# Optimization experiments

Hardware: AMD Instinct MI355X
Metric: run time of the kernel (lower is better)

The kernel has to match this reference:

```python
import jax, jax.numpy as jnp
import numpy as np

NUM_NODES = 50000
NUM_RELATIONS = 16
NUM_EDGES = 800000
HIDDEN = 64
NUM_CLASSES = 16


def setup_inputs() -> dict:
    key = jax.random.key(0)
    ks = jax.random.split(key, 8)
    edge_index = jax.random.randint(ks[0], (2, NUM_EDGES), 0, NUM_NODES, dtype=jnp.int32)
    edge_type = jax.random.randint(ks[1], (NUM_EDGES,), 0, NUM_RELATIONS, dtype=jnp.int32)
    node_emb = jax.random.normal(ks[2], (NUM_NODES, HIDDEN), dtype=jnp.float32) * 0.1
    W1 = jax.random.normal(ks[3], (NUM_RELATIONS, HIDDEN, HIDDEN), dtype=jnp.float32) * 0.1
    root1 = jax.random.normal(ks[4], (HIDDEN, HIDDEN), dtype=jnp.float32) * 0.1
    b1 = jnp.zeros((HIDDEN,), dtype=jnp.float32)
    W2 = jax.random.normal(ks[5], (NUM_RELATIONS, HIDDEN, NUM_CLASSES), dtype=jnp.float32) * 0.1
    root2 = jax.random.normal(ks[6], (HIDDEN, NUM_CLASSES), dtype=jnp.float32) * 0.1
    b2 = jnp.zeros((NUM_CLASSES,), dtype=jnp.float32)
    return {"edge_index": edge_index, "edge_type": edge_type, "node_emb": node_emb,
            "W1": W1, "root1": root1, "b1": b1, "W2": W2, "root2": root2, "b2": b2}


def rgcn_conv(x, src, dst, edge_type, W, root, bias, num_nodes):
    # PyG RGCNConv (aggr='mean', root_weight=True, bias=True, num_bases=None):
    # per relation r: transform all nodes, gather at src, scatter-MEAN at dst
    # (mean over edges of that relation per target node); sum over relations;
    # then add root transform and bias.
    out_dim = W.shape[-1]

    def body(acc, rw):
        W_r, r = rw
        h = x @ W_r                                   # [N, out]
        mask = (edge_type == r).astype(x.dtype)       # [E]
        msg = h[src] * mask[:, None]                  # [E, out]
        summed = jax.ops.segment_sum(msg, dst, num_segments=num_nodes)  # [N, out]
        cnt = jax.ops.segment_sum(mask, dst, num_segments=num_nodes)    # [N]
        mean = jnp.where(cnt[:, None] > 0, summed / jnp.maximum(cnt, 1.0)[:, None], 0.0)
        return acc + mean, None

    acc0 = jnp.zeros((num_nodes, out_dim), dtype=x.dtype)
    agg, _ = jax.lax.scan(body, acc0, (W, jnp.arange(W.shape[0])))
    return agg + x @ root + bias


def reference(edge_index, edge_type, node_emb, W1, root1, b1, W2, root2, b2):
    src, dst = edge_index[0], edge_index[1]
    n = node_emb.shape[0]
    x = rgcn_conv(node_emb, src, dst, edge_type, W1, root1, b1, n)
    x = jax.nn.relu(x)  # dropout p=0.0 -> identity
    x = rgcn_conv(x, src, dst, edge_type, W2, root2, b2, n)
    return x
```

## Files before the change

kernel.cpp:

```cpp
#include <hip/hip_runtime.h>
#include <hip/hip_bf16.h>

#define N_NODES 50000
#define NREL 16
#define HID 64
#define NCLS 16
#define NBKT (N_NODES * NREL)
#define SB 2048
#define NSB ((NBKT + SB - 1) / SB)
#define TILE 32
#define NTB ((N_NODES + TILE - 1) / TILE)
#define PGRID 256
#define XCHUNKS (N_NODES * HID / 8)
#define W1N (17 * HID * HID)
#define W2N (17 * NCLS * HID)

typedef __attribute__((ext_vector_type(8))) short bf16x8;
typedef __attribute__((ext_vector_type(4))) float f32x4;
typedef __attribute__((ext_vector_type(2))) int i32x2;

static __device__ __forceinline__ unsigned short f2bf(float f) {
    __hip_bfloat16 h = __float2bfloat16(f);
    return *reinterpret_cast<unsigned short*>(&h);
}
static __device__ __forceinline__ float bf2f(unsigned short u) {
    __hip_bfloat16 h;
    *reinterpret_cast<unsigned short*>(&h) = u;
    return __bfloat162float(h);
}

#define MFMA16(A, B, C) __builtin_amdgcn_mfma_f32_16x16x32_bf16((A), (B), (C), 0, 0, 0)

#define LD128A(D, P) \
    asm volatile("global_load_dwordx4 %0, %1, off" : "=v"(D) : "v"((const void*)(P)) : "memory")
#define LD64A(D, P) \
    asm volatile("global_load_dwordx2 %0, %1, off" : "=v"(D) : "v"((const void*)(P)) : "memory")
#define VWAIT0()                                           \
    do {                                                   \
        asm volatile("s_waitcnt vmcnt(0)" ::: "memory");   \
        __builtin_amdgcn_sched_barrier(0);                 \
    } while (0)


__global__ __launch_bounds__(256) void pre_k(const int* __restrict__ dstp,
                                             const int* __restrict__ et,
                                             int* __restrict__ bcnt, int E,
                                             const float* __restrict__ x,
                                             const float* __restrict__ W1,
                                             const float* __restrict__ root1,
                                             const float* __restrict__ W2,
                                             const float* __restrict__ root2,
                                             ushort* __restrict__ xb,
                                             ushort* __restrict__ WbT1,
                                             ushort* __restrict__ WbT2) {
    int eb = (E + 255) >> 8;
    if ((int)blockIdx.x < eb) {
        int i = blockIdx.x * 256 + threadIdx.x;
        if (i < E) atomicAdd(&bcnt[dstp[i] * NREL + et[i]], 1);
        return;
    }
    int i = (blockIdx.x - eb) * 256 + threadIdx.x;
    if (i < XCHUNKS) {
        float4 f0 = *(const float4*)(x + (size_t)i * 8);
        float4 f1 = *(const float4*)(x + (size_t)i * 8 + 4);
        bf16x8 o;
        o[0] = (short)f2bf(f0.x); o[1] = (short)f2bf(f0.y);
        o[2] = (short)f2bf(f0.z); o[3] = (short)f2bf(f0.w);
        o[4] = (short)f2bf(f1.x); o[5] = (short)f2bf(f1.y);
        o[6] = (short)f2bf(f1.z); o[7] = (short)f2bf(f1.w);
        *(bf16x8*)(xb + (size_t)i * 8) = o;
    } else {
        int j = i - XCHUNKS;
        if (j < W1N) {
            int t = j >> 12, rem = j & 4095, n = rem >> 6, k = rem & 63;
            float v = (t < 16) ? W1[(size_t)t * HID * HID + k * HID + n]
                               : root1[k * HID + n];
            WbT1[j] = f2bf(v);
        } else {
            int m = j - W1N;
            if (m < W2N) {
                int t = m >> 10, rem = m & 1023, n = rem >> 6, k = rem & 63;
                float v = (t < 16) ? W2[(size_t)t * HID * NCLS + k * NCLS + n]
                                   : root2[k * NCLS + n];
                WbT2[m] = f2bf(v);
            }
        }
    }
}

__global__ __launch_bounds__(256) void scan1_k(const int* __restrict__ bcnt,
                                               int* __restrict__ bsum) {
    int b = blockIdx.x, t = threadIdx.x;
    int base = b * SB + t * 8;
    int s = 0;
#pragma unroll
    for (int j = 0; j < 8; ++j)
        if (base + j < NBKT) s += bcnt[base + j];
#pragma unroll
    for (int off = 1; off < 64; off <<= 1) s += __shfl_xor(s, off, 64);
    __shared__ int ws[4];
    if ((t & 63) == 0) ws[t >> 6] = s;
    __syncthreads();
    if (t == 0) bsum[b] = ws[0] + ws[1] + ws[2] + ws[3];
}

__global__ __launch_bounds__(256) void scan23_k(int* __restrict__ bcnt,
                                                const int* __restrict__ bsum,
                                                int* __restrict__ cursor, int E) {
    int b = blockIdx.x, t = threadIdx.x;
    int ps = 0;
    for (int j = t; j < b; j += 256) ps += bsum[j];
#pragma unroll
    for (int off = 1; off < 64; off <<= 1) ps += __shfl_xor(ps, off, 64);
    __shared__ int wps[4];
    __shared__ int prefix;
    if ((t & 63) == 0) wps[t >> 6] = ps;
    __syncthreads();
    if (t == 0) prefix = wps[0] + wps[1] + wps[2] + wps[3];

    int base = b * SB + t * 8;
    int a[8];
    int s = 0;
#pragma unroll
    for (int j = 0; j < 8; ++j) {
        a[j] = (base + j < NBKT) ? bcnt[base + j] : 0;
        s += a[j];
    }
    __shared__ int ts[256];
    ts[t] = s;
    __syncthreads();
    int acc = s;
    for (int off = 1; off < 256; off <<= 1) {
        int u = (t >= off) ? ts[t - off] : 0;
        __syncthreads();
        acc += u;
        ts[t] = acc;
        __syncthreads();
    }
    int run = prefix + (acc - s);
#pragma unroll
    for (int j = 0; j < 8; ++j) {
        if (base + j < NBKT) {
            bcnt[base + j] = run;
            cursor[base + j] = run;
        }
        run += a[j];
    }
    if (b == 0 && t == 0) bcnt[NBKT] = E;
}

__global__ __launch_bounds__(256) void scat_k(const int* __restrict__ srcp,
                                              const int* __restrict__ dstp,
                                              const int* __restrict__ et,
                                              const int* __restrict__ rstart,
                                              int* __restrict__ cursor,
                                              int2* __restrict__ sedge, int E) {
    int i = blockIdx.x * 256 + threadIdx.x;
    if (i < E) {
        int r = et[i];
        int b = dstp[i] * NREL + r;
        int p = atomicAdd(&cursor[b], 1);
        float inv = 1.0f / (float)(rstart[b + 1] - rstart[b]);
        sedge[p] = make_int2(srcp[i] | (r << 16), __float_as_int(inv));
    }
}


#define RSTART_LOAD(T, LO, HI)                                                \
    do {                                                                      \
        int node_ = (T) * TILE + g;                                           \
        LO = 0; HI = 0;                                                       \
        if (node_ < N_NODES) {                                                \
            int b0_ = node_ * NREL + h * 8;                                   \
            LO = rstart[b0_];                                                 \
            HI = rstart[b0_ + 8];                                             \
        }                                                                     \
    } while (0)

#define DESC_ISSUE(LO, HI)                                                    \
    do {                                                                      \
        int dg_ = (HI) - (LO);                                                \
        int bs_ = dg_ > 0 ? (LO) : 0;                                         \
        int lt_ = dg_ > 0 ? (HI)-1 : 0;                                       \
        _Pragma("unroll") for (int j_ = 0; j_ < 16; ++j_) {                   \
            int ix_ = bs_ + j_;                                               \
            if (ix_ > lt_) ix_ = lt_;                                         \
            LD64A(d[j_], sedge + ix_);                                        \
        }                                                                     \
    } while (0)

#define FEAT_ISSUE()                                                          \
    do {                                                                      \
        _Pragma("unroll") for (int j_ = 0; j_ < 16; ++j_)                     \
            LD128A(v[j_], xcol + (size_t)(d[j_].x & 0xFFFF) * HID);           \
    } while (0)

#define GFLUSHX(ABP)                                                          \
    {                                                                         \
        bf16x8 o_;                                                            \
        o_[0] = (short)f2bf(acc_[0]); o_[1] = (short)f2bf(acc_[1]);           \
        o_[2] = (short)f2bf(acc_[2]); o_[3] = (short)f2bf(acc_[3]);           \
        o_[4] = (short)f2bf(acc_[4]); o_[5] = (short)f2bf(acc_[5]);           \
        o_[6] = (short)f2bf(acc_[6]); o_[7] = (short)f2bf(acc_[7]);           \
        *(bf16x8*)((ABP) + ((curRel_ * (TILE * 128) + rowoff) ^ swg)) = o_;   \
        acc_[0] = 0.f; acc_[1] = 0.f; acc_[2] = 0.f; acc_[3] = 0.f;           \
        acc_[4] = 0.f; acc_[5] = 0.f; acc_[6] = 0.f; acc_[7] = 0.f;           \
    }

#define CONSUME(ABP, LO, HI)                                                  \
    do {                                                                      \
        char* abp_ = (char*)(ABP);                                            \
        int deg_ = (HI) - (LO);                                               \
        const bf16x8 zz_ = {0, 0, 0, 0, 0, 0, 0, 0};                          \
        _Pragma("unroll") for (int r_ = 0; r_ < 8; ++r_)                      \
            *(bf16x8*)(abp_ + (((h * 8 + r_) * (TILE * 128) + rowoff) ^ swg)) = zz_; \
        float acc_[8] = {0.f, 0.f, 0.f, 0.f, 0.f, 0.f, 0.f, 0.f};             \
        int curRel_ = h * 8;                                                  \
        _Pragma("unroll") for (int j_ = 0; j_ < 16; ++j_) {                   \
            if (j_ < deg_) {                                                  \
                int rr_ = (d[j_].x >> 16) & 15;                               \
                if (rr_ != curRel_) { GFLUSHX(abp_); curRel_ = rr_; }         \
                float iv_ = __int_as_float(d[j_].y);                          \
                _Pragma("unroll") for (int q_ = 0; q_ < 8; ++q_)              \
                    acc_[q_] = fmaf(iv_, bf2f((unsigned short)v[j_][q_]), acc_[q_]); \
            }                                                                 \
        }                                                                     \
        for (int e_ = (LO) + 16; e_ < (HI); ++e_) {            \
            int2 m_ = sedge[e_];                                              \
            int rr_ = (m_.x >> 16) & 15;                                      \
            if (rr_ != curRel_) { GFLUSHX(abp_); curRel_ = rr_; }             \
            float iv_ = __int_as_float(m_.y);                                 \
            bf16x8 vv_ = *(const bf16x8*)(xcol + (size_t)(m_.x & 0xFFFF) * HID); \
            _Pragma("unroll") for (int q_ = 0; q_ < 8; ++q_)                  \
                acc_[q_] = fmaf(iv_, bf2f((unsigned short)vv_[q_]), acc_[q_]); \
        }                                                                     \
        if (deg_ > 0) GFLUSHX(abp_);                                          \
    } while (0)

__global__ __launch_bounds__(512, 2) void fuse1_k(const ushort* __restrict__ xb,
                                                  const int2* __restrict__ sedge,
                                                  const int* __restrict__ rstart,
                                                  const ushort* __restrict__ WbT1,
                                                  const float* __restrict__ b1,
                                                  ushort* __restrict__ X1b) {
    __shared__ bf16x8 Abuf[2][NREL * TILE * 8];
    __shared__ float P[4][TILE][16];
    int tid = threadIdx.x, bid = blockIdx.x;
    int wave = tid >> 6, lane = tid & 63;
    int mr = lane & 15, kq = lane >> 4;
    int cg = wave & 3, th = wave >> 2;
    int grp = tid >> 3, l8 = tid & 7;
    int g = grp & 31, h = grp >> 5;
    int swg = (g & 7) << 4;
    int rowoff = (g << 7) + (l8 << 4);
    const ushort* xcol = xb + l8 * 8;
    int sw = (mr & 7) << 4;
    int a00o = ((mr << 7) + (kq << 4)) ^ sw;
    int a01o = ((mr << 7) + 64 + (kq << 4)) ^ sw;
    int a10o = (((16 + mr) << 7) + (kq << 4)) ^ sw;
    int a11o = (((16 + mr) << 7) + 64 + (kq << 4)) ^ sw;

    const ushort* wbase = WbT1 + (cg * 16 + mr) * HID + kq * 8;
    bf16x8 w0[8], w1[8];
#pragma unroll
    for (int i = 0; i < 8; ++i) {
        w0[i] = *(const bf16x8*)(wbase + (th * 8 + i) * 4096);
        w1[i] = *(const bf16x8*)(wbase + (th * 8 + i) * 4096 + 32);
    }
    bf16x8 wr0 = *(const bf16x8*)(wbase + 16 * 4096);
    bf16x8 wr1 = *(const bf16x8*)(wbase + 16 * 4096 + 32);
    float4 bv = *(const float4*)(b1 + ((tid * 4) & 63));

    i32x2 d[16];
    bf16x8 v[16];

    int lo, hi;
    RSTART_LOAD(bid, lo, hi);
    DESC_ISSUE(lo, hi);
    VWAIT0();
    FEAT_ISSUE();
    VWAIT0();
    CONSUME(&Abuf[0][0], lo, hi);
    int cur = 0;

    for (int k = 0;; ++k) {
        int tile = bid + k * PGRID;
        int dst0 = tile * TILE;
        bool hasNext = (tile + PGRID) < NTB;
        int nlo = 0, nhi = 0;
        if (hasNext) RSTART_LOAD(tile + PGRID, nlo, nhi);
        __syncthreads();
        if (hasNext) DESC_ISSUE(nlo, nhi);
        int r0 = dst0 + mr;      if (r0 >= N_NODES) r0 = N_NODES - 1;
        int r1 = dst0 + 16 + mr; if (r1 >= N_NODES) r1 = N_NODES - 1;
        bf16x8 ra00, ra01, ra10, ra11;
        LD128A(ra00, xb + (size_t)r0 * HID + kq * 8);
        LD128A(ra01, xb + (size_t)r0 * HID + kq * 8 + 32);
        LD128A(ra10, xb + (size_t)r1 * HID + kq * 8);
        LD128A(ra11, xb + (size_t)r1 * HID + kq * 8 + 32);

        const char* Abase = (const char*)&Abuf[cur][0] + th * (8 * TILE * 128);
        f32x4 c0 = {0.f, 0.f, 0.f, 0.f}, c1 = {0.f, 0.f, 0.f, 0.f};
#pragma unroll
        for (int i = 0; i < 4; ++i) {
            const char* At = Abase + i * (TILE * 128);
            bf16x8 a00 = *(const bf16x8*)(At + a00o);
            bf16x8 a01 = *(const bf16x8*)(At + a01o);
            bf16x8 a10 = *(const bf16x8*)(At + a10o);
            bf16x8 a11 = *(const bf16x8*)(At + a11o);
            c0 = MFMA16(a00, w0[i], c0);
            c0 = MFMA16(a01, w1[i], c0);
            c1 = MFMA16(a10, w0[i], c1);
            c1 = MFMA16(a11, w1[i], c1);
        }
        VWAIT0();
        if (hasNext) FEAT_ISSUE();
#pragma unroll
        for (int i = 4; i < 8; ++i) {
            const char* At = Abase + i * (TILE * 128);
            bf16x8 a00 = *(const bf16x8*)(At + a00o);
            bf16x8 a01 = *(const bf16x8*)(At + a01o);
            bf16x8 a10 = *(const bf16x8*)(At + a10o);
            bf16x8 a11 = *(const bf16x8*)(At + a11o);
            c0 = MFMA16(a00, w0[i], c0);
            c0 = MFMA16(a01, w1[i], c0);
            c1 = MFMA16(a10, w0[i], c1);
            c1 = MFMA16(a11, w1[i], c1);
        }
        if (th) {
            c0 = MFMA16(ra00, wr0, c0);
            c0 = MFMA16(ra01, wr1, c0);
            c1 = MFMA16(ra10, wr0, c1);
            c1 = MFMA16(ra11, wr1, c1);
        }
        if (th == 0) {
#pragma unroll
            for (int j = 0; j < 4; ++j) {
                P[cg][kq * 4 + j][mr] = c0[j];
                P[cg][16 + kq * 4 + j][mr] = c1[j];
            }
        }
        __syncthreads();
        if (th == 1) {
#pragma unroll
            for (int j = 0; j < 4; ++j) {
                P[cg][kq * 4 + j][mr] += c0[j];
                P[cg][16 + kq * 4 + j][mr] += c1[j];
            }
        }
        __syncthreads();
        {
            int idx = tid * 4, row = idx >> 6, colb = idx & 63;
            int node = dst0 + row;
            if (node < N_NODES) {
                f32x4 pv = *(const f32x4*)&P[colb >> 4][row][colb & 15];
                ushort4 o;
                o.x = f2bf(fmaxf(pv[0] + bv.x, 0.f));
                o.y = f2bf(fmaxf(pv[1] + bv.y, 0.f));
                o.z = f2bf(fmaxf(pv[2] + bv.z, 0.f));
                o.w = f2bf(fmaxf(pv[3] + bv.w, 0.f));
                *(ushort4*)(X1b + (size_t)node * HID + colb) = o;
            }
        }
        if (!hasNext) break;
        VWAIT0();
        CONSUME(&Abuf[cur ^ 1][0], nlo, nhi);
        cur ^= 1;
    }
}


#define GFLUSH()                                                              \
    {                                                                         \
        bf16x8 o_;                                                            \
        o_[0] = (short)f2bf(acc[0]); o_[1] = (short)f2bf(acc[1]);             \
        o_[2] = (short)f2bf(acc[2]); o_[3] = (short)f2bf(acc[3]);             \
        o_[4] = (short)f2bf(acc[4]); o_[5] = (short)f2bf(acc[5]);             \
        o_[6] = (short)f2bf(acc[6]); o_[7] = (short)f2bf(acc[7]);             \
        *(bf16x8*)(Ab + ((curRel * (TILE * 128) + rowoff) ^ sw)) = o_;        \
        acc[0] = 0.f; acc[1] = 0.f; acc[2] = 0.f; acc[3] = 0.f;               \
        acc[4] = 0.f; acc[5] = 0.f; acc[6] = 0.f; acc[7] = 0.f;               \
    }

static __device__ __forceinline__ void gather_tile(char* Ab,
                                                   const ushort* __restrict__ ft,
                                                   const int2* __restrict__ sedge,
                                                   const int* __restrict__ rstart,
                                                   int dst0, int tid) {
    int g = tid >> 3, l8 = tid & 7;
    int node = dst0 + g;
    bool valid = node < N_NODES;

    int lo = 0, hi = 0;
    if (valid) {
        lo = rstart[node * NREL];
        hi = rstart[node * NREL + NREL];
    }
    int deg = hi - lo;
    int base = (deg > 0) ? lo : 0;
    int last = (deg > 0) ? hi - 1 : 0;

    int sw = (g & 7) << 4;
    int rowoff = (g << 7) + (l8 << 4);
    const bf16x8 zz = {0, 0, 0, 0, 0, 0, 0, 0};

    int2 d[32];
#pragma unroll
    for (int j = 0; j < 32; ++j) {
        int idx = base + j;
        if (idx > last) idx = last;
        d[j] = sedge[idx];
    }

#pragma unroll
    for (int t = 0; t < 16; ++t)
        *(bf16x8*)(Ab + ((t * (TILE * 128) + rowoff) ^ sw)) = zz;
    {
        bf16x8 v = zz;
        if (valid) v = *(const bf16x8*)(ft + (size_t)node * HID + l8 * 8);
        *(bf16x8*)(Ab + ((16 * (TILE * 128) + rowoff) ^ sw)) = v;
    }

    const ushort* xcol = ft + l8 * 8;
    bf16x8 v[32];
#pragma unroll
    for (int j = 0; j < 32; ++j)
        v[j] = *(const bf16x8*)(xcol + (size_t)(d[j].x & 0xFFFF) * HID);
    __builtin_amdgcn_sched_barrier(0);

    float acc[8] = {0.f, 0.f, 0.f, 0.f, 0.f, 0.f, 0.f, 0.f};
    int curRel = 0;
#pragma unroll
    for (int j = 0; j < 32; ++j) {
        if (j < deg) {
            int r_ = (d[j].x >> 16) & 15;
            if (r_ != curRel) {
                GFLUSH();
                curRel = r_;
            }
            float inv_ = __int_as_float(d[j].y);
#pragma unroll
            for (int q = 0; q < 8; ++q)
                acc[q] = fmaf(inv_, bf2f((unsigned short)v[j][q]), acc[q]);
        }
    }
    for (int e = lo + 32; e < hi; ++e) {
        int2 m = sedge[e];
        int r = (m.x >> 16) & 15;
        if (r != curRel) {
            GFLUSH();
            curRel = r;
        }
        float inv = __int_as_float(m.y);
        bf16x8 vv = *(const bf16x8*)(xcol + (size_t)(m.x & 0xFFFF) * HID);
#pragma unroll
        for (int q = 0; q < 8; ++q)
            acc[q] = fmaf(inv, bf2f((unsigned short)vv[q]), acc[q]);
    }
    if (deg > 0) GFLUSH();
}

__global__ __launch_bounds__(256, 2) void fuse2_k(const ushort* __restrict__ X1b,
                                                  const int2* __restrict__ sedge,
                                                  const int* __restrict__ rstart,
                                                  const ushort* __restrict__ WbT2,
                                                  const float* __restrict__ b2,
                                                  float* __restrict__ out) {
    __shared__ bf16x8 Abuf[17 * TILE * 8];
    __shared__ float P[4 * TILE * NCLS];
    char* Ab = (char*)Abuf;
    int tid = threadIdx.x;
    int dst0 = blockIdx.x * TILE;

    gather_tile(Ab, X1b, sedge, rstart, dst0, tid);

    int wave = tid >> 6, lane = tid & 63;
    int mr = lane & 15, kq = lane >> 4;
    f32x4 c0 = {0.f, 0.f, 0.f, 0.f}, c1 = {0.f, 0.f, 0.f, 0.f};
    const ushort* wb = WbT2 + mr * HID + kq * 8;
    int sw = (mr & 7) << 4;
    int a00o = ((mr << 7) + (kq << 4)) ^ sw;
    int a01o = ((mr << 7) + 64 + (kq << 4)) ^ sw;
    int a10o = (((16 + mr) << 7) + (kq << 4)) ^ sw;
    int a11o = (((16 + mr) << 7) + 64 + (kq << 4)) ^ sw;

    bf16x8 bk0 = *(const bf16x8*)(wb + wave * 1024);
    bf16x8 bk1 = *(const bf16x8*)(wb + wave * 1024 + 32);
    __syncthreads();

    for (int t = wave; t < 17; t += 4) {
        bf16x8 nb0 = bk0, nb1 = bk1;
        if (t + 4 < 17) {
            nb0 = *(const bf16x8*)(wb + (t + 4) * 1024);
            nb1 = *(const bf16x8*)(wb + (t + 4) * 1024 + 32);
        }
        const char* At = Ab + t * (TILE * 128);
        bf16x8 a00 = *(const bf16x8*)(At + a00o);
        bf16x8 a01 = *(const bf16x8*)(At + a01o);
        bf16x8 a10 = *(const bf16x8*)(At + a10o);
        bf16x8 a11 = *(const bf16x8*)(At + a11o);
        c0 = MFMA16(a00, bk0, c0);
        c0 = MFMA16(a01, bk1, c0);
        c1 = MFMA16(a10, bk0, c1);
        c1 = MFMA16(a11, bk1, c1);
        bk0 = nb0;
        bk1 = nb1;
    }
    float* Pw = P + wave * (TILE * NCLS);
#pragma unroll
    for (int j = 0; j < 4; ++j) {
        Pw[(kq * 4 + j) * NCLS + mr] = c0[j];
        Pw[(16 + kq * 4 + j) * NCLS + mr] = c1[j];
    }
    __syncthreads();

    int idx = tid * 2;
    int row = idx >> 4, c = idx & 15;
    float s0 = P[idx] + P[512 + idx] + P[1024 + idx] + P[1536 + idx] + b2[c];
    float s1 = P[idx + 1] + P[512 + idx + 1] + P[1024 + idx + 1] +
               P[1536 + idx + 1] + b2[c + 1];
    if (dst0 + row < N_NODES) {
        float2 o = make_float2(s0, s1);
        *(float2*)(out + (size_t)(dst0 + row) * NCLS + c) = o;
    }
}

extern "C" void kernel_launch(void* const* d_in, const int* in_sizes, int n_in,
                              void* d_out, int out_size, void* d_ws, size_t ws_size,
                              hipStream_t stream) {
    const int* ei    = (const int*)d_in[0];
    const int* et    = (const int*)d_in[1];
    const float* x   = (const float*)d_in[2];
    const float* W1  = (const float*)d_in[3];
    const float* r1  = (const float*)d_in[4];
    const float* b1  = (const float*)d_in[5];
    const float* W2  = (const float*)d_in[6];
    const float* r2  = (const float*)d_in[7];
    const float* b2  = (const float*)d_in[8];
    float* out = (float*)d_out;

    int E = in_sizes[0] / 2;
    const int* srcp = ei;
    const int* dstp = ei + E;

    int*    bcnt   = (int*)d_ws;
    int*    cursor = bcnt + (NBKT + 20);
    int*    bsum   = cursor + NBKT;
    int2*   sedge  = (int2*)(bsum + 512);
    ushort* WbT1   = (ushort*)(sedge + E);
    ushort* WbT2   = WbT1 + W1N;
    ushort* xb     = WbT2 + W2N;
    ushort* X1b    = xb + (size_t)N_NODES * HID;
    int*    rstart = bcnt;

    hipMemsetAsync(bcnt, 0, (NBKT + 20) * sizeof(int), stream);

    int eb = (E + 255) / 256;
    int cvtThreads = XCHUNKS + W1N + W2N;
    int cvtBlocks = (cvtThreads + 255) / 256;

    pre_k<<<eb + cvtBlocks, 256, 0, stream>>>(dstp, et, bcnt, E,
                                              x, W1, r1, W2, r2, xb, WbT1, WbT2);
    scan1_k<<<NSB, 256, 0, stream>>>(bcnt, bsum);
    scan23_k<<<NSB, 256, 0, stream>>>(bcnt, bsum, cursor, E);
    scat_k<<<eb, 256, 0, stream>>>(srcp, dstp, et, rstart, cursor, sedge, E);

    fuse1_k<<<PGRID, 512, 0, stream>>>(xb, sedge, rstart, WbT1, b1, X1b);
    fuse2_k<<<NTB, 256, 0, stream>>>(X1b, sedge, rstart, WbT2, b2, out);
}
```

Before: 259.8 us.

## Merge CSR build into one cooperative kernel with grid syncs and rank-based scatter

```diff
diff --git a/kernel.cpp b/kernel.cpp
--- a/kernel.cpp
+++ b/kernel.cpp
@@ -1,5 +1,8 @@
 #include <hip/hip_runtime.h>
 #include <hip/hip_bf16.h>
+#include <hip/hip_cooperative_groups.h>
+
+namespace cg = cooperative_groups;
 
 #define N_NODES 50000
 #define NREL 16
@@ -11,6 +14,7 @@
 #define TILE 32
 #define NTB ((N_NODES + TILE - 1) / TILE)
 #define PGRID 256
+#define COOPG 1024
 #define XCHUNKS (N_NODES * HID / 8)
 #define W1N (17 * HID * HID)
 #define W2N (17 * NCLS * HID)
@@ -42,9 +46,123 @@
     } while (0)
 
 
+__global__ __launch_bounds__(256) void coop_pre_k(
+        const int* __restrict__ srcp, const int* __restrict__ dstp,
+        const int* __restrict__ et, int* __restrict__ bcnt,
+        int* __restrict__ rank, int E,
+        const float* __restrict__ x, const float* __restrict__ W1,
+        const float* __restrict__ root1, const float* __restrict__ W2,
+        const float* __restrict__ root2, ushort* __restrict__ xb,
+        ushort* __restrict__ WbT1, ushort* __restrict__ WbT2,
+        int* __restrict__ bsum, int2* __restrict__ sedge) {
+    __shared__ int ts[256];
+    __shared__ int ws[4];
+    int tid = threadIdx.x, bid = blockIdx.x;
+    int gsz = gridDim.x * 256;
+    int gtid = bid * 256 + tid;
+
+    for (int i = gtid; i < NBKT + 20; i += gsz) bcnt[i] = 0;
+    cg::this_grid().sync();
+
+    for (int i = gtid; i < E; i += gsz) {
+        int b = dstp[i] * NREL + et[i];
+        rank[i] = atomicAdd(&bcnt[b], 1);
+    }
+    for (int i = gtid; i < XCHUNKS + W1N + W2N; i += gsz) {
+        if (i < XCHUNKS) {
+            float4 f0 = *(const float4*)(x + (size_t)i * 8);
+            float4 f1 = *(const float4*)(x + (size_t)i * 8 + 4);
+            bf16x8 o;
+            o[0] = (short)f2bf(f0.x); o[1] = (short)f2bf(f0.y);
+            o[2] = (short)f2bf(f0.z); o[3] = (short)f2bf(f0.w);
+            o[4] = (short)f2bf(f1.x); o[5] = (short)f2bf(f1.y);
+            o[6] = (short)f2bf(f1.z); o[7] = (short)f2bf(f1.w);
+            *(bf16x8*)(xb + (size_t)i * 8) = o;
+        } else {
+            int j = i - XCHUNKS;
+            if (j < W1N) {
+                int t = j >> 12, rem = j & 4095, n = rem >> 6, k = rem & 63;
+                float v = (t < 16) ? W1[(size_t)t * HID * HID + k * HID + n]
+                                   : root1[k * HID + n];
+                WbT1[j] = f2bf(v);
+            } else {
+                int m = j - W1N;
+                int t = m >> 10, rem = m & 1023, n = rem >> 6, k = rem & 63;
+                float v = (t < 16) ? W2[(size_t)t * HID * NCLS + k * NCLS + n]
+                                   : root2[k * NCLS + n];
+                WbT2[m] = f2bf(v);
+            }
+        }
+    }
+    cg::this_grid().sync();
+
+    for (int c = bid; c < NSB; c += gridDim.x) {
+        int base = c * SB + tid * 8;
+        int s = 0;
+#pragma unroll
+        for (int j = 0; j < 8; ++j)
+            if (base + j < NBKT) s += bcnt[base + j];
+#pragma unroll
+        for (int off = 1; off < 64; off <<= 1) s += __shfl_xor(s, off, 64);
+        if ((tid & 63) == 0) ws[tid >> 6] = s;
+        __syncthreads();
+        if (tid == 0) bsum[c] = ws[0] + ws[1] + ws[2] + ws[3];
+        __syncthreads();
+    }
+    cg::this_grid().sync();
+
+    for (int c = bid; c < NSB; c += gridDim.x) {
+        int ps = 0;
+        for (int j = tid; j < c; j += 256) ps += bsum[j];
+#pragma unroll
+        for (int off = 1; off < 64; off <<= 1) ps += __shfl_xor(ps, off, 64);
+        if ((tid & 63) == 0) ws[tid >> 6] = ps;
+        __syncthreads();
+        int prefix = ws[0] + ws[1] + ws[2] + ws[3];
+
+        int base = c * SB + tid * 8;
+        int a[8];
+        int s = 0;
+#pragma unroll
+        for (int j = 0; j < 8; ++j) {
+            a[j] = (base + j < NBKT) ? bcnt[base + j] : 0;
+            s += a[j];
+        }
+        ts[tid] = s;
+        __syncthreads();
+        int acc = s;
+        for (int off = 1; off < 256; off <<= 1) {
+            int u = (tid >= off) ? ts[tid - off] : 0;
+            __syncthreads();
+            acc += u;
+            ts[tid] = acc;
+            __syncthreads();
+        }
+        int run = prefix + (acc - s);
+#pragma unroll
+        for (int j = 0; j < 8; ++j) {
+            if (base + j < NBKT) bcnt[base + j] = run;
+            run += a[j];
+        }
+        __syncthreads();
+    }
+    if (gtid == 0) bcnt[NBKT] = E;
+    cg::this_grid().sync();
+
+    for (int i = gtid; i < E; i += gsz) {
+        int r = et[i];
+        int b = dstp[i] * NREL + r;
+        int lo = bcnt[b], hi = bcnt[b + 1];
+        float inv = 1.0f / (float)(hi - lo);
+        sedge[lo + rank[i]] = make_int2(srcp[i] | (r << 16), __float_as_int(inv));
+    }
+}
+
+
 __global__ __launch_bounds__(256) void pre_k(const int* __restrict__ dstp,
                                              const int* __restrict__ et,
-                                             int* __restrict__ bcnt, int E,
+                                             int* __restrict__ bcnt,
+                                             int* __restrict__ rank, int E,
                                              const float* __restrict__ x,
                                              const float* __restrict__ W1,
                                              const float* __restrict__ root1,
@@ -56,7 +174,10 @@
     int eb = (E + 255) >> 8;
     if ((int)blockIdx.x < eb) {
         int i = blockIdx.x * 256 + threadIdx.x;
-        if (i < E) atomicAdd(&bcnt[dstp[i] * NREL + et[i]], 1);
+        if (i < E) {
+            int b = dstp[i] * NREL + et[i];
+            rank[i] = atomicAdd(&bcnt[b], 1);
+        }
         return;
     }
     int i = (blockIdx.x - eb) * 256 + threadIdx.x;
@@ -104,20 +225,28 @@
     if (t == 0) bsum[b] = ws[0] + ws[1] + ws[2] + ws[3];
 }
 
-__global__ __launch_bounds__(256) void scan23_k(int* __restrict__ bcnt,
-                                                const int* __restrict__ bsum,
-                                                int* __restrict__ cursor, int E) {
+__global__ __launch_bounds__(512) void scan2_k(int* __restrict__ bsum,
+                                               int* __restrict__ rstart, int E) {
+    __shared__ int ts[512];
+    int t = threadIdx.x;
+    int v = (t < NSB) ? bsum[t] : 0;
+    ts[t] = v;
+    __syncthreads();
+    int acc = v;
+    for (int off = 1; off < 512; off <<= 1) {
+        int u = (t >= off) ? ts[t - off] : 0;
+        __syncthreads();
+        acc += u;
+        ts[t] = acc;
+        __syncthreads();
+    }
+    if (t < NSB) bsum[t] = acc - v;
+    if (t == 0) rstart[NBKT] = E;
+}
+
+__global__ __launch_bounds__(256) void scan3_k(int* __restrict__ bcnt,
+                                               const int* __restrict__ bsum) {
     int b = blockIdx.x, t = threadIdx.x;
-    int ps = 0;
-    for (int j = t; j < b; j += 256) ps += bsum[j];
-#pragma unroll
-    for (int off = 1; off < 64; off <<= 1) ps += __shfl_xor(ps, off, 64);
-    __shared__ int wps[4];
-    __shared__ int prefix;
-    if ((t & 63) == 0) wps[t >> 6] = ps;
-    __syncthreads();
-    if (t == 0) prefix = wps[0] + wps[1] + wps[2] + wps[3];
-
     int base = b * SB + t * 8;
     int a[8];
     int s = 0;
@@ -137,31 +266,27 @@
         ts[t] = acc;
         __syncthreads();
     }
-    int run = prefix + (acc - s);
+    int run = bsum[b] + (acc - s);
 #pragma unroll
     for (int j = 0; j < 8; ++j) {
-        if (base + j < NBKT) {
-            bcnt[base + j] = run;
-            cursor[base + j] = run;
-        }
+        if (base + j < NBKT) bcnt[base + j] = run;
         run += a[j];
     }
-    if (b == 0 && t == 0) bcnt[NBKT] = E;
 }
 
 __global__ __launch_bounds__(256) void scat_k(const int* __restrict__ srcp,
                                               const int* __restrict__ dstp,
                                               const int* __restrict__ et,
+                                              const int* __restrict__ rank,
                                               const int* __restrict__ rstart,
-                                              int* __restrict__ cursor,
                                               int2* __restrict__ sedge, int E) {
     int i = blockIdx.x * 256 + threadIdx.x;
     if (i < E) {
         int r = et[i];
         int b = dstp[i] * NREL + r;
-        int p = atomicAdd(&cursor[b], 1);
-        float inv = 1.0f / (float)(rstart[b + 1] - rstart[b]);
-        sedge[p] = make_int2(srcp[i] | (r << 16), __float_as_int(inv));
+        int lo = rstart[b], hi = rstart[b + 1];
+        float inv = 1.0f / (float)(hi - lo);
+        sedge[lo + rank[i]] = make_int2(srcp[i] | (r << 16), __float_as_int(inv));
     }
 }
 
@@ -248,7 +373,7 @@
     int tid = threadIdx.x, bid = blockIdx.x;
     int wave = tid >> 6, lane = tid & 63;
     int mr = lane & 15, kq = lane >> 4;
-    int cg = wave & 3, th = wave >> 2;
+    int cg_ = wave & 3, th = wave >> 2;
     int grp = tid >> 3, l8 = tid & 7;
     int g = grp & 31, h = grp >> 5;
     int swg = (g & 7) << 4;
@@ -260,7 +385,7 @@
     int a10o = (((16 + mr) << 7) + (kq << 4)) ^ sw;
     int a11o = (((16 + mr) << 7) + 64 + (kq << 4)) ^ sw;
 
-    const ushort* wbase = WbT1 + (cg * 16 + mr) * HID + kq * 8;
+    const ushort* wbase = WbT1 + (cg_ * 16 + mr) * HID + kq * 8;
     bf16x8 w0[8], w1[8];
 #pragma unroll
     for (int i = 0; i < 8; ++i) {
@@ -336,16 +461,16 @@
         if (th == 0) {
 #pragma unroll
             for (int j = 0; j < 4; ++j) {
-                P[cg][kq * 4 + j][mr] = c0[j];
-                P[cg][16 + kq * 4 + j][mr] = c1[j];
+                P[cg_][kq * 4 + j][mr] = c0[j];
+                P[cg_][16 + kq * 4 + j][mr] = c1[j];
             }
         }
         __syncthreads();
         if (th == 1) {
 #pragma unroll
             for (int j = 0; j < 4; ++j) {
-                P[cg][kq * 4 + j][mr] += c0[j];
-                P[cg][16 + kq * 4 + j][mr] += c1[j];
+                P[cg_][kq * 4 + j][mr] += c0[j];
+                P[cg_][16 + kq * 4 + j][mr] += c1[j];
             }
         }
         __syncthreads();
@@ -544,8 +669,8 @@
     const int* dstp = ei + E;
 
     int*    bcnt   = (int*)d_ws;
-    int*    cursor = bcnt + (NBKT + 20);
-    int*    bsum   = cursor + NBKT;
+    int*    rank   = bcnt + (NBKT + 20);
+    int*    bsum   = rank + E;
     int2*   sedge  = (int2*)(bsum + 512);
     ushort* WbT1   = (ushort*)(sedge + E);
     ushort* WbT2   = WbT1 + W1N;
@@ -553,17 +678,27 @@
     ushort* X1b    = xb + (size_t)N_NODES * HID;
     int*    rstart = bcnt;
 
-    hipMemsetAsync(bcnt, 0, (NBKT + 20) * sizeof(int), stream);
-
     int eb = (E + 255) / 256;
     int cvtThreads = XCHUNKS + W1N + W2N;
     int cvtBlocks = (cvtThreads + 255) / 256;
 
-    pre_k<<<eb + cvtBlocks, 256, 0, stream>>>(dstp, et, bcnt, E,
-                                              x, W1, r1, W2, r2, xb, WbT1, WbT2);
-    scan1_k<<<NSB, 256, 0, stream>>>(bcnt, bsum);
-    scan23_k<<<NSB, 256, 0, stream>>>(bcnt, bsum, cursor, E);
-    scat_k<<<eb, 256, 0, stream>>>(srcp, dstp, et, rstart, cursor, sedge, E);
+    void* kargs[] = {(void*)&srcp, (void*)&dstp, (void*)&et,
+                     (void*)&bcnt, (void*)&rank, (void*)&E,
+                     (void*)&x, (void*)&W1, (void*)&r1, (void*)&W2, (void*)&r2,
+                     (void*)&xb, (void*)&WbT1, (void*)&WbT2,
+                     (void*)&bsum, (void*)&sedge};
+    hipError_t cerr = hipLaunchCooperativeKernel(
+        reinterpret_cast<const void*>(&coop_pre_k), dim3(COOPG), dim3(256),
+        kargs, 0u, stream);
+    if (cerr != hipSuccess) {
+        hipMemsetAsync(bcnt, 0, (NBKT + 20) * sizeof(int), stream);
+        pre_k<<<eb + cvtBlocks, 256, 0, stream>>>(dstp, et, bcnt, rank, E,
+                                                  x, W1, r1, W2, r2, xb, WbT1, WbT2);
+        scan1_k<<<NSB, 256, 0, stream>>>(bcnt, bsum);
+        scan2_k<<<1, 512, 0, stream>>>(bsum, rstart, E);
+        scan3_k<<<NSB, 256, 0, stream>>>(bcnt, bsum);
+        scat_k<<<eb, 256, 0, stream>>>(srcp, dstp, et, rank, rstart, sedge, E);
+    }
 
     fuse1_k<<<PGRID, 512, 0, stream>>>(xb, sedge, rstart, WbT1, b1, X1b);
     fuse2_k<<<NTB, 256, 0, stream>>>(X1b, sedge, rstart, WbT2, b2, out);
```

Result: slower. 643.8 us (+147.8%).

## Capture per-edge rank in counting pass and split block scan into separate kernel

Applied to the files above, without the earlier changes.

```diff
diff --git a/kernel.cpp b/kernel.cpp
--- a/kernel.cpp
+++ b/kernel.cpp
@@ -44,7 +44,8 @@
 
 __global__ __launch_bounds__(256) void pre_k(const int* __restrict__ dstp,
                                              const int* __restrict__ et,
-                                             int* __restrict__ bcnt, int E,
+                                             int* __restrict__ bcnt,
+                                             int* __restrict__ rank, int E,
                                              const float* __restrict__ x,
                                              const float* __restrict__ W1,
                                              const float* __restrict__ root1,
@@ -56,7 +57,10 @@
     int eb = (E + 255) >> 8;
     if ((int)blockIdx.x < eb) {
         int i = blockIdx.x * 256 + threadIdx.x;
-        if (i < E) atomicAdd(&bcnt[dstp[i] * NREL + et[i]], 1);
+        if (i < E) {
+            int b = dstp[i] * NREL + et[i];
+            rank[i] = atomicAdd(&bcnt[b], 1);
+        }
         return;
     }
     int i = (blockIdx.x - eb) * 256 + threadIdx.x;
@@ -104,20 +108,28 @@
     if (t == 0) bsum[b] = ws[0] + ws[1] + ws[2] + ws[3];
 }
 
-__global__ __launch_bounds__(256) void scan23_k(int* __restrict__ bcnt,
-                                                const int* __restrict__ bsum,
-                                                int* __restrict__ cursor, int E) {
+__global__ __launch_bounds__(512) void scan2_k(int* __restrict__ bsum,
+                                               int* __restrict__ rstart, int E) {
+    __shared__ int ts[512];
+    int t = threadIdx.x;
+    int v = (t < NSB) ? bsum[t] : 0;
+    ts[t] = v;
+    __syncthreads();
+    int acc = v;
+    for (int off = 1; off < 512; off <<= 1) {
+        int u = (t >= off) ? ts[t - off] : 0;
+        __syncthreads();
+        acc += u;
+        ts[t] = acc;
+        __syncthreads();
+    }
+    if (t < NSB) bsum[t] = acc - v;
+    if (t == 0) rstart[NBKT] = E;
+}
+
+__global__ __launch_bounds__(256) void scan3_k(int* __restrict__ bcnt,
+                                               const int* __restrict__ bsum) {
     int b = blockIdx.x, t = threadIdx.x;
-    int ps = 0;
-    for (int j = t; j < b; j += 256) ps += bsum[j];
-#pragma unroll
-    for (int off = 1; off < 64; off <<= 1) ps += __shfl_xor(ps, off, 64);
-    __shared__ int wps[4];
-    __shared__ int prefix;
-    if ((t & 63) == 0) wps[t >> 6] = ps;
-    __syncthreads();
-    if (t == 0) prefix = wps[0] + wps[1] + wps[2] + wps[3];
-
     int base = b * SB + t * 8;
     int a[8];
     int s = 0;
@@ -137,31 +149,27 @@
         ts[t] = acc;
         __syncthreads();
     }
-    int run = prefix + (acc - s);
+    int run = bsum[b] + (acc - s);
 #pragma unroll
     for (int j = 0; j < 8; ++j) {
-        if (base + j < NBKT) {
-            bcnt[base + j] = run;
-            cursor[base + j] = run;
-        }
+        if (base + j < NBKT) bcnt[base + j] = run;
         run += a[j];
     }
-    if (b == 0 && t == 0) bcnt[NBKT] = E;
 }
 
 __global__ __launch_bounds__(256) void scat_k(const int* __restrict__ srcp,
                                               const int* __restrict__ dstp,
                                               const int* __restrict__ et,
+                                              const int* __restrict__ rank,
                                               const int* __restrict__ rstart,
-                                              int* __restrict__ cursor,
                                               int2* __restrict__ sedge, int E) {
     int i = blockIdx.x * 256 + threadIdx.x;
     if (i < E) {
         int r = et[i];
         int b = dstp[i] * NREL + r;
-        int p = atomicAdd(&cursor[b], 1);
-        float inv = 1.0f / (float)(rstart[b + 1] - rstart[b]);
-        sedge[p] = make_int2(srcp[i] | (r << 16), __float_as_int(inv));
+        int lo = rstart[b], hi = rstart[b + 1];
+        float inv = 1.0f / (float)(hi - lo);
+        sedge[lo + rank[i]] = make_int2(srcp[i] | (r << 16), __float_as_int(inv));
     }
 }
 
@@ -248,7 +256,7 @@
     int tid = threadIdx.x, bid = blockIdx.x;
     int wave = tid >> 6, lane = tid & 63;
     int mr = lane & 15, kq = lane >> 4;
-    int cg = wave & 3, th = wave >> 2;
+    int cg_ = wave & 3, th = wave >> 2;
     int grp = tid >> 3, l8 = tid & 7;
     int g = grp & 31, h = grp >> 5;
     int swg = (g & 7) << 4;
@@ -260,7 +268,7 @@
     int a10o = (((16 + mr) << 7) + (kq << 4)) ^ sw;
     int a11o = (((16 + mr) << 7) + 64 + (kq << 4)) ^ sw;
 
-    const ushort* wbase = WbT1 + (cg * 16 + mr) * HID + kq * 8;
+    const ushort* wbase = WbT1 + (cg_ * 16 + mr) * HID + kq * 8;
     bf16x8 w0[8], w1[8];
 #pragma unroll
     for (int i = 0; i < 8; ++i) {
@@ -336,16 +344,16 @@
         if (th == 0) {
 #pragma unroll
             for (int j = 0; j < 4; ++j) {
-                P[cg][kq * 4 + j][mr] = c0[j];
-                P[cg][16 + kq * 4 + j][mr] = c1[j];
+                P[cg_][kq * 4 + j][mr] = c0[j];
+                P[cg_][16 + kq * 4 + j][mr] = c1[j];
             }
         }
         __syncthreads();
         if (th == 1) {
 #pragma unroll
             for (int j = 0; j < 4; ++j) {
-                P[cg][kq * 4 + j][mr] += c0[j];
-                P[cg][16 + kq * 4 + j][mr] += c1[j];
+                P[cg_][kq * 4 + j][mr] += c0[j];
+                P[cg_][16 + kq * 4 + j][mr] += c1[j];
             }
         }
         __syncthreads();
@@ -543,14 +551,14 @@
     const int* srcp = ei;
     const int* dstp = ei + E;
 
-    int*    bcnt   = (int*)d_ws;
-    int*    cursor = bcnt + (NBKT + 20);
-    int*    bsum   = cursor + NBKT;
-    int2*   sedge  = (int2*)(bsum + 512);
-    ushort* WbT1   = (ushort*)(sedge + E);
-    ushort* WbT2   = WbT1 + W1N;
-    ushort* xb     = WbT2 + W2N;
-    ushort* X1b    = xb + (size_t)N_NODES * HID;
+    int*    bcnt  = (int*)d_ws;
+    int*    rank  = bcnt + (NBKT + 20);
+    int*    bsum  = rank + E;
+    int2*   sedge = (int2*)(bsum + 512);
+    ushort* WbT1  = (ushort*)(sedge + E);
+    ushort* WbT2  = WbT1 + W1N;
+    ushort* xb    = WbT2 + W2N;
+    ushort* X1b   = xb + (size_t)N_NODES * HID;
     int*    rstart = bcnt;
 
     hipMemsetAsync(bcnt, 0, (NBKT + 20) * sizeof(int), stream);
@@ -559,11 +567,12 @@
     int cvtThreads = XCHUNKS + W1N + W2N;
     int cvtBlocks = (cvtThreads + 255) / 256;
 
-    pre_k<<<eb + cvtBlocks, 256, 0, stream>>>(dstp, et, bcnt, E,
+    pre_k<<<eb + cvtBlocks, 256, 0, stream>>>(dstp, et, bcnt, rank, E,
                                               x, W1, r1, W2, r2, xb, WbT1, WbT2);
     scan1_k<<<NSB, 256, 0, stream>>>(bcnt, bsum);
-    scan23_k<<<NSB, 256, 0, stream>>>(bcnt, bsum, cursor, E);
-    scat_k<<<eb, 256, 0, stream>>>(srcp, dstp, et, rstart, cursor, sedge, E);
+    scan2_k<<<1, 512, 0, stream>>>(bsum, rstart, E);
+    scan3_k<<<NSB, 256, 0, stream>>>(bcnt, bsum);
+    scat_k<<<eb, 256, 0, stream>>>(srcp, dstp, et, rank, rstart, sedge, E);
 
     fuse1_k<<<PGRID, 512, 0, stream>>>(xb, sedge, rstart, WbT1, b1, X1b);
     fuse2_k<<<NTB, 256, 0, stream>>>(X1b, sedge, rstart, WbT2, b2, out);
```

Result: faster. 236.3 us (-9.0%).
